# Optimization experiments

Measured on AMD Instinct MI355X. Metric: run time of the kernel, lower is better.

## Reference

```python
import jax, jax.numpy as jnp
import numpy as np

B, D, C, P = 1024, 768, 150, 64  # batch, in_feats, num_labels, proj2 dim
POS_M, NEG_M = 0.7, 1.4


def setup_inputs() -> dict:
    key = jax.random.key(0)
    ks = jax.random.split(key, 8)
    return {
        "x": jax.random.normal(ks[0], (B, D), jnp.float32),
        "lb": jax.random.randint(ks[1], (B,), 0, C + 1),
        "mem": jax.random.normal(ks[2], (C, D), jnp.float32),
        "fc_w": jax.random.normal(ks[3], (2 * D, 2 * D), jnp.float32) * 0.02,
        "fc_b": jnp.zeros((2 * D,), jnp.float32),
        "p1_w": jax.random.normal(ks[4], (1, 2 * D), jnp.float32) * 0.02,
        "p1_b": jnp.zeros((1,), jnp.float32),
        "p2_w": jax.random.normal(ks[5], (P, 2 * D), jnp.float32) * 0.02,
        "p2_b": jnp.zeros((P,), jnp.float32),
    }


def reference(x, lb, mem, fc_w, fc_b, p1_w, p1_b, p2_w, p2_b):
    d = x.shape[1]
    # cat([a, b], 1) @ fc_w.T == a @ Wx.T + b @ Wm.T  (exact split of the linear)
    Wx, Wm = fc_w[:, :d], fc_w[:, d:]
    xh = x @ Wx.T + fc_b                                # [B, 2D]

    # --- get_logit ---
    seen_h = jax.nn.relu(xh[:, None, :] + mem @ Wm.T)   # [B, C, 2D]
    seen = jnp.einsum('bce,e->bc', seen_h, p1_w[0]) + p1_b[0]   # [B, C]
    uh = jax.nn.relu(xh)                                # cat([x, zeros]) path
    unseen = uh @ p1_w.T + p1_b                         # [B, 1]
    logits = jnp.concatenate([seen, unseen], axis=1)    # [B, C+1]

    # --- masked log-softmax losses (pos_adapte) ---
    labels = jax.nn.one_hot(lb, C + 1, dtype=jnp.float32)
    th = jnp.zeros_like(labels).at[:, -1].set(1.0)
    labels = labels.at[:, -1].set(0.0)
    p_mask = labels + th
    n_mask = 1.0 - labels
    BIG = 1e30
    loss1 = -(jax.nn.log_softmax(logits - (1.0 - p_mask) * BIG, -1) * labels).sum(1)
    loss2 = -(jax.nn.log_softmax(logits - (1.0 - n_mask) * BIG, -1) * th).sum(1)
    loss_cls = (loss1 + loss2).mean()

    # --- metric loss on unseen embedding ---
    u = uh @ p2_w.T + p2_b                              # [B, 64]
    u = u / jnp.maximum(jnp.linalg.norm(u, axis=1, keepdims=True), 1e-12)
    sq_n = (u * u).sum(1)
    sq = sq_n[:, None] + sq_n[None, :] - 2.0 * (u @ u.T)
    err = sq <= 0.0
    dist = jnp.sqrt(jnp.clip(sq, 1e-16, None)) * (~err).astype(u.dtype)
    same = lb[:, None] == lb[None, :]
    eye = jnp.eye(dist.shape[0], dtype=bool)
    pos = (same & ~eye).astype(dist.dtype)
    neg = (~same).astype(dist.dtype)
    pos_l = (jax.nn.relu(dist - POS_M) * pos).sum() / jnp.maximum(pos.sum(), 1.0)
    neg_l = (jax.nn.relu(NEG_M - dist) * neg).sum() / jnp.maximum(neg.sum(), 1.0)

    return loss_cls + pos_l + neg_l
```

## Files before the change

kernel.cpp:

```cpp
#include <hip/hip_runtime.h>
#include <math.h>

#define B_    1024
#define D_    768
#define C_    150
#define P_    64
#define TWOD  1536
#define NCLS  151
#define CPAD  256

#define ECHUNKS 16
#define ECHUNK  96

#define GSTR  72
#define GBUF  (64 * GSTR)
#define NKT   (D_ / 64)
#define USTRU 120
#define USTR  72
#define XSTR  192

#define NBLK  512

#define OFF_MH      0
#define OFF_XH      (OFF_MH + (C_ * TWOD) / 2)
#define OFF_PARTIAL (OFF_XH + (B_ * TWOD) / 2)
#define OFF_UHF     (OFF_PARTIAL + ECHUNKS * B_ * CPAD)
#define OFF_SQN     (OFF_UHF + (B_ * P_) / 2)
#define OFF_CLS     (OFF_SQN + B_)
#define OFF_PAIR    (OFF_CLS + B_)

typedef __bf16    bfx8   __attribute__((ext_vector_type(8)));
typedef _Float16  fp16x8 __attribute__((ext_vector_type(8)));
typedef _Float16  h2v    __attribute__((ext_vector_type(2)));
typedef float     f32x4  __attribute__((ext_vector_type(4)));

__device__ int g_arr[8 * 16];
__device__ int g_gen[32 * 16];

__device__ inline ushort f2bf(float f) {
    union { float f; unsigned u; } c; c.f = f;
    unsigned r = c.u + 0x7fffu + ((c.u >> 16) & 1u);
    return (ushort)(r >> 16);
}
__device__ inline ushort f2h(float f) {
    _Float16 h = (_Float16)f;
    return __builtin_bit_cast(ushort, h);
}
__device__ inline uint4 pack_bf8(float4 a, float4 b) {
    uint4 r;
    r.x = (unsigned)f2bf(a.x) | ((unsigned)f2bf(a.y) << 16);
    r.y = (unsigned)f2bf(a.z) | ((unsigned)f2bf(a.w) << 16);
    r.z = (unsigned)f2bf(b.x) | ((unsigned)f2bf(b.y) << 16);
    r.w = (unsigned)f2bf(b.z) | ((unsigned)f2bf(b.w) << 16);
    return r;
}
__device__ inline uint4 pack_h8(float4 a, float4 b) {
    uint4 r;
    r.x = (unsigned)f2h(a.x) | ((unsigned)f2h(a.y) << 16);
    r.y = (unsigned)f2h(a.z) | ((unsigned)f2h(a.w) << 16);
    r.z = (unsigned)f2h(b.x) | ((unsigned)f2h(b.y) << 16);
    r.w = (unsigned)f2h(b.z) | ((unsigned)f2h(b.w) << 16);
    return r;
}
__device__ inline unsigned addrelu2(unsigned a, unsigned m) {
    h2v s = __builtin_bit_cast(h2v, a) + __builtin_bit_cast(h2v, m);
    h2v z = {(_Float16)0.f, (_Float16)0.f};
    s = __builtin_elementwise_max(s, z);
    return __builtin_bit_cast(unsigned, s);
}
__device__ inline unsigned relu2(unsigned a) {
    h2v s = __builtin_bit_cast(h2v, a);
    h2v z = {(_Float16)0.f, (_Float16)0.f};
    s = __builtin_elementwise_max(s, z);
    return __builtin_bit_cast(unsigned, s);
}
__device__ inline float dot2acc(unsigned a, unsigned b, float c) {
    return __builtin_amdgcn_fdot2(__builtin_bit_cast(h2v, a),
                                  __builtin_bit_cast(h2v, b), c, false);
}

__device__ __forceinline__ void st_wt_u16(ushort* p, unsigned v) {
    asm volatile("global_store_short %0, %1, off sc0 sc1"
                 :: "v"(p), "v"(v) : "memory");
}
__device__ __forceinline__ void st_wt_f32(float* p, float v) {
    asm volatile("global_store_dword %0, %1, off sc0 sc1"
                 :: "v"(p), "v"(v) : "memory");
}
__device__ __forceinline__ void st_wt_f32x4(float* p, f32x4 v) {
    asm volatile("global_store_dwordx4 %0, %1, off sc0 sc1"
                 :: "v"(p), "v"(v) : "memory");
}

__device__ __forceinline__ void grid_barrier(int G0, int b)
{
    asm volatile("s_waitcnt vmcnt(0)" ::: "memory");
    __syncthreads();
    if (threadIdx.x == 0) {
        const int target = G0 + b;
        __hip_atomic_fetch_add(&g_arr[(blockIdx.x & 7) * 16], 1,
                               __ATOMIC_RELAXED, __HIP_MEMORY_SCOPE_AGENT);
        if (blockIdx.x == 0) {
            const int starget = NBLK * target;
            for (;;) {
                int s = 0;
#pragma unroll
                for (int k = 0; k < 8; ++k)
                    s += __hip_atomic_load(&g_arr[k * 16], __ATOMIC_RELAXED,
                                           __HIP_MEMORY_SCOPE_AGENT);
                if (s - starget >= 0) break;
                __builtin_amdgcn_s_sleep(1);
            }
#pragma unroll
            for (int r = 0; r < 32; ++r)
                __hip_atomic_store(&g_gen[r * 16], target, __ATOMIC_RELAXED,
                                   __HIP_MEMORY_SCOPE_AGENT);
        } else {
            int* myg = &g_gen[(blockIdx.x & 31) * 16];
            while (__hip_atomic_load(myg, __ATOMIC_RELAXED,
                                     __HIP_MEMORY_SCOPE_AGENT) - target < 0)
                __builtin_amdgcn_s_sleep(4);
        }
        asm volatile("" ::: "memory");
    }
    __syncthreads();
}

__device__ __forceinline__ void phase_gemm(
    int id, char* smemc,
    const float* __restrict__ x, const float* __restrict__ mem,
    const float* __restrict__ fc_w, const float* __restrict__ fc_b,
    ushort* __restrict__ xh, ushort* __restrict__ mh)
{
    if (id >= 456) return;
    ushort* As = (ushort*)smemc;
    ushort* Bs = (ushort*)(smemc + 2 * GBUF * 2);
    const int t = threadIdx.x;

    const float* A; ushort* Out; int M, m0, n0, koff; bool xblk;
    if (id < 384) {
        xblk = true;  A = x;    Out = xh; M = B_;
        m0 = (id & 15) * 64; n0 = (id >> 4) * 64; koff = 0;
    } else {
        int q = id - 384;
        xblk = false; A = mem;  Out = mh; M = C_;
        m0 = (q % 3) * 64; n0 = (q / 3) * 64; koff = D_;
    }

    const int wave = t >> 6, lane = t & 63;
    const int wm = wave * 16;
    const int fm = lane & 15, quad = lane >> 4;

    const int row_a = t >> 2, qa = (t & 3) * 16;
    const int ar = min(m0 + row_a, M - 1);
    const float* Arow = A + (size_t)ar * D_ + qa;
    const float* Brow = fc_w + (size_t)(n0 + row_a) * TWOD + koff + qa;
    const int lw = row_a * GSTR + qa;

    f32x4 acc[4];
#pragma unroll
    for (int j = 0; j < 4; ++j) {
        float bv = xblk ? fc_b[n0 + j * 16 + fm] : 0.f;
        acc[j] = (f32x4){bv, bv, bv, bv};
    }

    float4 pa0 = *(const float4*)(Arow);
    float4 pa1 = *(const float4*)(Arow + 4);
    float4 pa2 = *(const float4*)(Arow + 8);
    float4 pa3 = *(const float4*)(Arow + 12);
    float4 pb0 = *(const float4*)(Brow);
    float4 pb1 = *(const float4*)(Brow + 4);
    float4 pb2 = *(const float4*)(Brow + 8);
    float4 pb3 = *(const float4*)(Brow + 12);

    for (int kt = 0; kt < NKT; ++kt) {
        ushort* Ad = As + (kt & 1) * GBUF;
        ushort* Bd = Bs + (kt & 1) * GBUF;
        *(uint4*)&Ad[lw]     = pack_bf8(pa0, pa1);
        *(uint4*)&Ad[lw + 8] = pack_bf8(pa2, pa3);
        *(uint4*)&Bd[lw]     = pack_bf8(pb0, pb1);
        *(uint4*)&Bd[lw + 8] = pack_bf8(pb2, pb3);
        __syncthreads();
        if (kt + 1 < NKT) {
            const int k1 = (kt + 1) * 64;
            pa0 = *(const float4*)(Arow + k1);
            pa1 = *(const float4*)(Arow + k1 + 4);
            pa2 = *(const float4*)(Arow + k1 + 8);
            pa3 = *(const float4*)(Arow + k1 + 12);
            pb0 = *(const float4*)(Brow + k1);
            pb1 = *(const float4*)(Brow + k1 + 4);
            pb2 = *(const float4*)(Brow + k1 + 8);
            pb3 = *(const float4*)(Brow + k1 + 12);
        }
#pragma unroll
        for (int ks = 0; ks < 2; ++ks) {
            bfx8 af = *(const bfx8*)&Ad[(wm + fm) * GSTR + ks * 32 + quad * 8];
#pragma unroll
            for (int j = 0; j < 4; ++j) {
                bfx8 bf = *(const bfx8*)&Bd[(j * 16 + fm) * GSTR + ks * 32 + quad * 8];
                acc[j] = __builtin_amdgcn_mfma_f32_16x16x32_bf16(
                    af, bf, acc[j], 0, 0, 0);
            }
        }
    }

#pragma unroll
    for (int j = 0; j < 4; ++j)
#pragma unroll
        for (int r = 0; r < 4; ++r) {
            int row = m0 + wm + quad * 4 + r;
            int col = n0 + j * 16 + fm;
            if (row < M)
                st_wt_u16(&Out[(size_t)row * TWOD + col],
                          (unsigned)f2h(acc[j][r]));
        }
}

__device__ __forceinline__ void phase_fused(
    int id, char* smem,
    const ushort* __restrict__ xh, const ushort* __restrict__ mh,
    const float* __restrict__ p1w, const float* __restrict__ p2w,
    float* __restrict__ partial)
{
    const int t  = threadIdx.x;
    const int b0 = (id & 7) * 128;
    const int y  = (id >> 3) & 3;
    const int z  = id >> 5;
    const int e0 = z * ECHUNK;

    if (y == 3) {
        ushort* Au = (ushort*)smem;
        ushort* Wu = (ushort*)(smem + 30720);
        const int wave = t >> 6, lane = t & 63;
        const int fm = lane & 15, quad = lane >> 4;

        {
            const int row = t >> 1, kh = (t & 1) * 48;
            const ushort* src = xh + (size_t)(b0 + row) * TWOD + e0 + kh;
            uint4 v[6];
#pragma unroll
            for (int i = 0; i < 6; ++i) v[i] = *(const uint4*)&src[i * 8];
#pragma unroll
            for (int i = 0; i < 6; ++i) {
                v[i].x = relu2(v[i].x); v[i].y = relu2(v[i].y);
                v[i].z = relu2(v[i].z); v[i].w = relu2(v[i].w);
                *(uint4*)&Au[row * USTRU + kh + i * 8] = v[i];
            }
        }
        {
            const int row = t >> 2, ks = (t & 3) * 24;
            const float* pw = p2w + (size_t)row * TWOD + e0 + ks;
#pragma unroll
            for (int i = 0; i < 3; ++i) {
                float4 lo = *(const float4*)&pw[i * 8];
                float4 hi = *(const float4*)&pw[i * 8 + 4];
                *(uint4*)&Wu[row * USTRU + ks + i * 8] = pack_h8(lo, hi);
            }
        }
        __syncthreads();

        f32x4 uacc[2][4];
#pragma unroll
        for (int i = 0; i < 2; ++i)
#pragma unroll
            for (int j = 0; j < 4; ++j) uacc[i][j] = (f32x4){0.f, 0.f, 0.f, 0.f};
#pragma unroll
        for (int k0 = 0; k0 < ECHUNK; k0 += 32) {
            fp16x8 af[2], bff[4];
#pragma unroll
            for (int i = 0; i < 2; ++i)
                af[i] = *(const fp16x8*)&Au[(wave * 32 + i * 16 + fm) * USTRU + k0 + quad * 8];
#pragma unroll
            for (int j = 0; j < 4; ++j)
                bff[j] = *(const fp16x8*)&Wu[(j * 16 + fm) * USTRU + k0 + quad * 8];
#pragma unroll
            for (int i = 0; i < 2; ++i)
#pragma unroll
                for (int j = 0; j < 4; ++j)
                    uacc[i][j] = __builtin_amdgcn_mfma_f32_16x16x32_f16(
                        af[i], bff[j], uacc[i][j], 0, 0, 0);
        }
#pragma unroll
        for (int i = 0; i < 2; ++i)
#pragma unroll
            for (int j = 0; j < 4; ++j)
#pragma unroll
                for (int r = 0; r < 4; ++r) {
                    int row = b0 + wave * 32 + i * 16 + quad * 4 + r;
                    st_wt_f32(&partial[((size_t)z * B_ + row) * CPAD + 192 + j * 16 + fm],
                              uacc[i][j][r]);
                }
        return;
    }

    unsigned* xT = (unsigned*)smem;
    unsigned* mT = (unsigned*)(smem + 36864);
    unsigned* wT = (unsigned*)(smem + 49152);
    const int c0 = y * 64;
    const int tm = t & 15, tn = t >> 4;

    {
        const int row = t >> 1, ph = (t & 1) * 48;
        const int rowo = row + ((row >> 3) << 2);
        const ushort* src = xh + (size_t)(b0 + row) * TWOD + e0 + ph;
        uint4 v[6];
#pragma unroll
        for (int i = 0; i < 6; ++i) v[i] = *(const uint4*)&src[i * 8];
#pragma unroll
        for (int i = 0; i < 6; ++i) {
            const int ep = (t & 1) * 24 + i * 4;
            xT[(ep + 0) * XSTR + rowo] = v[i].x;
            xT[(ep + 1) * XSTR + rowo] = v[i].y;
            xT[(ep + 2) * XSTR + rowo] = v[i].z;
            xT[(ep + 3) * XSTR + rowo] = v[i].w;
        }
    }
    {
        const int col = t & 63, seg = t >> 6;
        const int gc  = c0 + col;
        uint4 v[3];
        if (gc < C_) {
            const ushort* src = mh + (size_t)gc * TWOD + e0 + seg * 24;
#pragma unroll
            for (int i = 0; i < 3; ++i) v[i] = *(const uint4*)&src[i * 8];
        } else {
#pragma unroll
            for (int i = 0; i < 3; ++i) v[i] = make_uint4(0, 0, 0, 0);
        }
#pragma unroll
        for (int i = 0; i < 3; ++i) {
            const int ep = seg * 12 + i * 4;
            mT[(ep + 0) * 64 + col] = v[i].x;
            mT[(ep + 1) * 64 + col] = v[i].y;
            mT[(ep + 2) * 64 + col] = v[i].z;
            mT[(ep + 3) * 64 + col] = v[i].w;
        }
    }
    if (t < 12) {
        float4 lo = *(const float4*)&p1w[e0 + t * 8];
        float4 hi = *(const float4*)&p1w[e0 + t * 8 + 4];
        uint4 v = pack_h8(lo, hi);
        wT[t * 4 + 0] = v.x; wT[t * 4 + 1] = v.y;
        wT[t * 4 + 2] = v.z; wT[t * 4 + 3] = v.w;
    }
    __syncthreads();

    float acc[8][4] = {};
#pragma unroll 4
    for (int ep = 0; ep < 48; ++ep) {
        uint4 a0 = *(const uint4*)&xT[ep * XSTR + tm * 12];
        uint4 a1 = *(const uint4*)&xT[ep * XSTR + tm * 12 + 4];
        uint4 mj = *(const uint4*)&mT[ep * 64 + tn * 4];
        const unsigned wv = wT[ep];
        const unsigned aa[8] = {a0.x, a0.y, a0.z, a0.w, a1.x, a1.y, a1.z, a1.w};
        const unsigned mm[4] = {mj.x, mj.y, mj.z, mj.w};
#pragma unroll
        for (int i = 0; i < 8; ++i)
#pragma unroll
            for (int j = 0; j < 4; ++j)
                acc[i][j] = dot2acc(addrelu2(aa[i], mm[j]), wv, acc[i][j]);
    }

#pragma unroll
    for (int i = 0; i < 8; ++i) {
        const int gb = b0 + tm * 8 + i;
        f32x4 v = {acc[i][0], acc[i][1], acc[i][2], acc[i][3]};
        st_wt_f32x4(&partial[((size_t)z * B_ + gb) * CPAD + c0 + tn * 4], v);
    }
}

__device__ __forceinline__ void phase_reduce(
    char* smemc,
    const float* __restrict__ partial,
    const float* __restrict__ p1b, const float* __restrict__ p2b,
    const int* __restrict__ lb,
    ushort* __restrict__ uhf, float* __restrict__ sqn,
    float* __restrict__ clsbuf)
{
    float* sval = (float*)smemc;
    const int t = threadIdx.x;
    for (int b = blockIdx.x; b < B_; b += NBLK) {
        float v = 0.f;
#pragma unroll
        for (int z = 0; z < ECHUNKS; ++z)
            v += partial[((size_t)z * B_ + b) * CPAD + t];
        if (t < NCLS)       v += p1b[0];
        else if (t >= 192)  v += p2b[t - 192];

        sval[t] = v;
        __syncthreads();

        if (t < 64) {
            float uv = sval[192 + t];
            float s = uv * uv;
#pragma unroll
            for (int off = 32; off; off >>= 1) s += __shfl_xor(s, off);
            float inv = 1.f / fmaxf(sqrtf(s), 1e-12f);
            st_wt_u16(&uhf[(size_t)b * P_ + t], (unsigned)f2h(uv * inv));
            if (t == 0) st_wt_f32(&sqn[b], s * inv * inv);

            const int l = lb[b];
            float mx = -1e30f;
            for (int j = t; j < NCLS; j += 64)
                if (!(j == l && l < C_)) mx = fmaxf(mx, sval[j]);
#pragma unroll
            for (int off = 32; off; off >>= 1) mx = fmaxf(mx, __shfl_xor(mx, off));
            float se = 0.f;
            for (int j = t; j < NCLS; j += 64)
                if (!(j == l && l < C_)) se += expf(sval[j] - mx);
#pragma unroll
            for (int off = 32; off; off >>= 1) se += __shfl_xor(se, off);

            if (t == 0) {
                float l150  = sval[C_];
                float loss2 = mx + logf(se) - l150;
                float loss1 = 0.f;
                if (l < C_) {
                    float a  = sval[l];
                    float m2 = fmaxf(a, l150);
                    loss1 = m2 - a + logf(expf(a - m2) + expf(l150 - m2));
                }
                st_wt_f32(&clsbuf[b], loss1 + loss2);
            }
        }
        __syncthreads();
    }
}

__device__ __forceinline__ void phase_pair(
    int id, char* smemc,
    const ushort* __restrict__ uhf, const float* __restrict__ sqn,
    const int* __restrict__ lb, float* __restrict__ pairpart)
{
    ushort* ui_s = (ushort*)smemc;
    ushort* uj_s = (ushort*)(smemc + 9216);
    float*  sni  = (float*)(smemc + 18432);
    float*  snj  = (float*)(smemc + 18688);
    int*    li   = (int*)(smemc + 18944);
    int*    lj   = (int*)(smemc + 19200);
    float*  red  = (float*)(smemc + 19456);

    const int t  = threadIdx.x;
    const int i0 = (id & 15) * 64, j0 = (id >> 4) * 64;

    for (int idx = t; idx < 512; idx += 256) {
        int row = idx >> 3, ch = (idx & 7) * 8;
        *(uint4*)&ui_s[row * USTR + ch] =
            *(const uint4*)&uhf[(size_t)(i0 + row) * P_ + ch];
        *(uint4*)&uj_s[row * USTR + ch] =
            *(const uint4*)&uhf[(size_t)(j0 + row) * P_ + ch];
    }
    if (t < 64)       { sni[t] = sqn[i0 + t]; li[t] = lb[i0 + t]; }
    else if (t < 128) { int q = t - 64; snj[q] = sqn[j0 + q]; lj[q] = lb[j0 + q]; }
    __syncthreads();

    const int wave = t >> 6, lane = t & 63;
    const int n = lane & 15, quad = lane >> 4;
    const int iw = wave * 16;

    const fp16x8 af0 = *(const fp16x8*)&ui_s[(iw + n) * USTR + quad * 8];
    const fp16x8 af1 = *(const fp16x8*)&ui_s[(iw + n) * USTR + quad * 8 + 32];

    f32x4 acc[4];
#pragma unroll
    for (int jt = 0; jt < 4; ++jt) {
        const fp16x8 bf0 = *(const fp16x8*)&uj_s[(jt * 16 + n) * USTR + quad * 8];
        const fp16x8 bf1 = *(const fp16x8*)&uj_s[(jt * 16 + n) * USTR + quad * 8 + 32];
        acc[jt] = __builtin_amdgcn_mfma_f32_16x16x32_f16(
            af0, bf0, (f32x4){0.f, 0.f, 0.f, 0.f}, 0, 0, 0);
        acc[jt] = __builtin_amdgcn_mfma_f32_16x16x32_f16(
            af1, bf1, acc[jt], 0, 0, 0);
    }

    float ps = 0.f, pc = 0.f, ns = 0.f, nc = 0.f;
#pragma unroll
    for (int jt = 0; jt < 4; ++jt)
#pragma unroll
        for (int r = 0; r < 4; ++r) {
            const int il = iw + quad * 4 + r;
            const int jl = jt * 16 + n;
            float sq = sni[il] + snj[jl] - 2.f * acc[jt][r];
            float dist = sq > 0.f ? sqrtf(fmaxf(sq, 1e-16f)) : 0.f;
            bool same = (li[il] == lj[jl]);
            if (same) {
                if (i0 + il != j0 + jl) { ps += fmaxf(dist - 0.7f, 0.f); pc += 1.f; }
            } else {
                ns += fmaxf(1.4f - dist, 0.f); nc += 1.f;
            }
        }

#pragma unroll
    for (int off = 32; off; off >>= 1) {
        ps += __shfl_xor(ps, off); pc += __shfl_xor(pc, off);
        ns += __shfl_xor(ns, off); nc += __shfl_xor(nc, off);
    }
    if (lane == 0) { red[0 * 4 + wave] = ps; red[1 * 4 + wave] = pc;
                     red[2 * 4 + wave] = ns; red[3 * 4 + wave] = nc; }
    __syncthreads();
    if (t == 0) {
        f32x4 v;
        v[0] = red[0] + red[1] + red[2] + red[3];
        v[1] = red[4] + red[5] + red[6] + red[7];
        v[2] = red[8] + red[9] + red[10] + red[11];
        v[3] = red[12] + red[13] + red[14] + red[15];
        st_wt_f32x4(&pairpart[(size_t)id * 4], v);
    }
}

__device__ __forceinline__ void phase_final(
    char* smemc,
    const float* __restrict__ clsbuf, const float* __restrict__ pairpart,
    float* __restrict__ out)
{
    float* red = (float*)smemc;
    const int t = threadIdx.x;
    float c = clsbuf[t] + clsbuf[t + 256] + clsbuf[t + 512] + clsbuf[t + 768];
    float4 pp = *(const float4*)&pairpart[(size_t)t * 4];
    float ps = pp.x, pc = pp.y, ns = pp.z, nc = pp.w;
#pragma unroll
    for (int off = 32; off; off >>= 1) {
        c  += __shfl_xor(c, off);
        ps += __shfl_xor(ps, off); pc += __shfl_xor(pc, off);
        ns += __shfl_xor(ns, off); nc += __shfl_xor(nc, off);
    }
    const int wave = t >> 6, lane = t & 63;
    if (lane == 0) { red[0 * 4 + wave] = c; red[1 * 4 + wave] = ps;
                     red[2 * 4 + wave] = pc; red[3 * 4 + wave] = ns;
                     red[4 * 4 + wave] = nc; }
    __syncthreads();
    if (t == 0) {
        float C = 0.f, PS = 0.f, PC = 0.f, NS = 0.f, NC = 0.f;
#pragma unroll
        for (int w = 0; w < 4; ++w) {
            C += red[0 * 4 + w]; PS += red[1 * 4 + w]; PC += red[2 * 4 + w];
            NS += red[3 * 4 + w]; NC += red[4 * 4 + w];
        }
        out[0] = C / (float)B_ + PS / fmaxf(PC, 1.f) + NS / fmaxf(NC, 1.f);
    }
}

__global__ __launch_bounds__(256, 2) void mega(
    const float* __restrict__ x, const int* __restrict__ lb,
    const float* __restrict__ mem, const float* __restrict__ fc_w,
    const float* __restrict__ fc_b, const float* __restrict__ p1w,
    const float* __restrict__ p1b, const float* __restrict__ p2w,
    const float* __restrict__ p2b,
    float* ws, float* out)
{
    __shared__ __align__(16) char smem[49344];

    ushort* mh       = (ushort*)(ws + OFF_MH);
    ushort* xh       = (ushort*)(ws + OFF_XH);
    float*  partial  = ws + OFF_PARTIAL;
    ushort* uhf      = (ushort*)(ws + OFF_UHF);
    float*  sqn      = ws + OFF_SQN;
    float*  clsbuf   = ws + OFF_CLS;
    float*  pairpart = ws + OFF_PAIR;

    const int id = blockIdx.x;

    int G0 = 0;
    if (threadIdx.x == 0) {
        G0 = __hip_atomic_load(&g_gen[(blockIdx.x & 31) * 16],
                               __ATOMIC_RELAXED, __HIP_MEMORY_SCOPE_AGENT);
        asm volatile("s_waitcnt vmcnt(0)" ::: "memory");
    }

    phase_gemm(id, smem, x, mem, fc_w, fc_b, xh, mh);
    grid_barrier(G0, 1);
    phase_fused(id, smem, xh, mh, p1w, p2w, partial);
    grid_barrier(G0, 2);
    phase_reduce(smem, partial, p1b, p2b, lb, uhf, sqn, clsbuf);
    grid_barrier(G0, 3);
    if (id < 256) phase_pair(id, smem, uhf, sqn, lb, pairpart);

    asm volatile("s_waitcnt vmcnt(0)" ::: "memory");
    __syncthreads();
    if (threadIdx.x == 0) {
        __hip_atomic_fetch_add(&g_arr[(blockIdx.x & 7) * 16], 1,
                               __ATOMIC_RELAXED, __HIP_MEMORY_SCOPE_AGENT);
    }
    if (blockIdx.x == 0) {
        if (threadIdx.x == 0) {
            const int starget = NBLK * (G0 + 4);
            for (;;) {
                int s = 0;
#pragma unroll
                for (int k = 0; k < 8; ++k)
                    s += __hip_atomic_load(&g_arr[k * 16], __ATOMIC_RELAXED,
                                           __HIP_MEMORY_SCOPE_AGENT);
                if (s - starget >= 0) break;
                __builtin_amdgcn_s_sleep(1);
            }
#pragma unroll
            for (int r = 0; r < 32; ++r)
                __hip_atomic_store(&g_gen[r * 16], G0 + 4, __ATOMIC_RELAXED,
                                   __HIP_MEMORY_SCOPE_AGENT);
        }
        asm volatile("" ::: "memory");
        __syncthreads();
        phase_final(smem, clsbuf, pairpart, out);
    }
}

extern "C" void kernel_launch(void* const* d_in, const int* in_sizes, int n_in,
                              void* d_out, int out_size, void* d_ws, size_t ws_size,
                              hipStream_t stream)
{
    const float* x    = (const float*)d_in[0];
    const int*   lb   = (const int*)d_in[1];
    const float* mem  = (const float*)d_in[2];
    const float* fc_w = (const float*)d_in[3];
    const float* fc_b = (const float*)d_in[4];
    const float* p1w  = (const float*)d_in[5];
    const float* p1b  = (const float*)d_in[6];
    const float* p2w  = (const float*)d_in[7];
    const float* p2b  = (const float*)d_in[8];

    float* ws = (float*)d_ws;

    mega<<<NBLK, 256, 0, stream>>>(x, lb, mem, fc_w, fc_b,
                                   p1w, p1b, p2w, p2b, ws, (float*)d_out);
}
```

Measured before the change: 131.5 us.

## Replace first grid barrier with per-tile dataflow flags between GEMM and fused phase

Each GEMM block publishes a per-tile generation flag after its writes drain, and each fused-phase block spins only on the specific xh/mh tiles it reads, instead of waiting at a full grid barrier. The generation counter bookkeeping drops from four barriers to three. This lets fused work start as soon as its inputs are ready, reducing barrier stall and tail imbalance. The cost is more fine-grained polling traffic and a reliance on relaxed atomics plus vmcnt waits for visibility.

Result: slower. 134.5 us (+2.3%).

```diff
diff --git a/kernel.cpp b/kernel.cpp
--- a/kernel.cpp
+++ b/kernel.cpp
@@ -36,6 +36,7 @@
 
 __device__ int g_arr[8 * 16];
 __device__ int g_gen[32 * 16];
+__device__ int g_flag[456];
 
 __device__ inline ushort f2bf(float f) {
     union { float f; unsigned u; } c; c.f = f;
@@ -127,7 +128,7 @@
 }
 
 __device__ __forceinline__ void phase_gemm(
-    int id, char* smemc,
+    int id, int G0, char* smemc,
     const float* __restrict__ x, const float* __restrict__ mem,
     const float* __restrict__ fc_w, const float* __restrict__ fc_b,
     ushort* __restrict__ xh, ushort* __restrict__ mh)
@@ -214,10 +215,16 @@
                 st_wt_u16(&Out[(size_t)row * TWOD + col],
                           (unsigned)f2h(acc[j][r]));
         }
+
+    asm volatile("s_waitcnt vmcnt(0)" ::: "memory");
+    __syncthreads();
+    if (t == 0)
+        __hip_atomic_store(&g_flag[id], G0 + 1, __ATOMIC_RELAXED,
+                           __HIP_MEMORY_SCOPE_AGENT);
 }
 
 __device__ __forceinline__ void phase_fused(
-    int id, char* smem,
+    int id, int G0, char* smem,
     const ushort* __restrict__ xh, const ushort* __restrict__ mh,
     const float* __restrict__ p1w, const float* __restrict__ p2w,
     float* __restrict__ partial)
@@ -227,6 +234,27 @@
     const int y  = (id >> 3) & 3;
     const int z  = id >> 5;
     const int e0 = z * ECHUNK;
+
+    {
+        const int mt0 = (id & 7) * 2;
+        const int nt0 = e0 >> 6;
+        const int nt1 = (e0 + ECHUNK - 1) >> 6;
+        int depid = -1;
+        if (t < 4) {
+            depid = (mt0 + (t & 1)) + 16 * ((t >> 1) ? nt1 : nt0);
+        } else if (y < 3 && t < 10) {
+            const int q = t - 4;
+            depid = 384 + (q >> 1) + 3 * ((q & 1) ? nt1 : nt0);
+        }
+        if (depid >= 0) {
+            const int target = G0 + 1;
+            while (__hip_atomic_load(&g_flag[depid], __ATOMIC_RELAXED,
+                                     __HIP_MEMORY_SCOPE_AGENT) - target < 0)
+                __builtin_amdgcn_s_sleep(2);
+        }
+        asm volatile("" ::: "memory");
+        __syncthreads();
+    }
 
     if (y == 3) {
         ushort* Au = (ushort*)smem;
@@ -548,6 +576,7 @@
     float* ws, float* out)
 {
     __shared__ __align__(16) char smem[49344];
+    __shared__ int G0s;
 
     ushort* mh       = (ushort*)(ws + OFF_MH);
     ushort* xh       = (ushort*)(ws + OFF_XH);
@@ -559,19 +588,18 @@
 
     const int id = blockIdx.x;
 
-    int G0 = 0;
     if (threadIdx.x == 0) {
-        G0 = __hip_atomic_load(&g_gen[(blockIdx.x & 31) * 16],
-                               __ATOMIC_RELAXED, __HIP_MEMORY_SCOPE_AGENT);
-        asm volatile("s_waitcnt vmcnt(0)" ::: "memory");
-    }
-
-    phase_gemm(id, smem, x, mem, fc_w, fc_b, xh, mh);
+        G0s = __hip_atomic_load(&g_gen[(blockIdx.x & 31) * 16],
+                                __ATOMIC_RELAXED, __HIP_MEMORY_SCOPE_AGENT);
+    }
+    __syncthreads();
+    const int G0 = G0s;
+
+    phase_gemm(id, G0, smem, x, mem, fc_w, fc_b, xh, mh);
+    phase_fused(id, G0, smem, xh, mh, p1w, p2w, partial);
     grid_barrier(G0, 1);
-    phase_fused(id, smem, xh, mh, p1w, p2w, partial);
+    phase_reduce(smem, partial, p1b, p2b, lb, uhf, sqn, clsbuf);
     grid_barrier(G0, 2);
-    phase_reduce(smem, partial, p1b, p2b, lb, uhf, sqn, clsbuf);
-    grid_barrier(G0, 3);
     if (id < 256) phase_pair(id, smem, uhf, sqn, lb, pairpart);
 
     asm volatile("s_waitcnt vmcnt(0)" ::: "memory");
@@ -582,7 +610,7 @@
     }
     if (blockIdx.x == 0) {
         if (threadIdx.x == 0) {
-            const int starget = NBLK * (G0 + 4);
+            const int starget = NBLK * (G0 + 3);
             for (;;) {
                 int s = 0;
 #pragma unroll
@@ -594,7 +622,7 @@
             }
 #pragma unroll
             for (int r = 0; r < 32; ++r)
-                __hip_atomic_store(&g_gen[r * 16], G0 + 4, __ATOMIC_RELAXED,
+                __hip_atomic_store(&g_gen[r * 16], G0 + 3, __ATOMIC_RELAXED,
                                    __HIP_MEMORY_SCOPE_AGENT);
         }
         asm volatile("" ::: "memory");
```
